# Kernel optimization log

Hardware: AMD Instinct MI355X
Metric: run time of the kernel (lower is better)

The kernel has to match this reference:

```python
import jax, jax.numpy as jnp
import numpy as np

B, T, C, H = 2, 2048, 1024, 16
HS = C // H  # 64
EPS = 1e-5


def layer_norm(x, w, b):
    mu = jnp.mean(x, axis=-1, keepdims=True)
    var = jnp.var(x, axis=-1, keepdims=True)
    return (x - mu) * jax.lax.rsqrt(var + EPS) * w + b


def setup_inputs() -> dict:
    key = jax.random.key(0)
    ks = jax.random.split(key, 16)
    s_c = 1.0 / np.sqrt(C)
    s_f = 1.0 / np.sqrt(4 * C)
    u = lambda k, shape, s: jax.random.uniform(k, shape, jnp.float32, -s, s)
    return {
        "x": jax.random.normal(ks[0], (B, T, C), jnp.float32),
        # per-head Q/K/V Linears stacked over heads: [H, C, HS], bias [H, HS]
        "Wq": u(ks[1], (H, C, HS), s_c), "bq": u(ks[2], (H, HS), s_c),
        "Wk": u(ks[3], (H, C, HS), s_c), "bk": u(ks[4], (H, HS), s_c),
        "Wv": u(ks[5], (H, C, HS), s_c), "bv": u(ks[6], (H, HS), s_c),
        "Wp": u(ks[7], (C, C), s_c), "bp": u(ks[8], (C,), s_c),
        "W1": u(ks[9], (C, 4 * C), s_c), "b1": u(ks[10], (4 * C,), s_c),
        "W2": u(ks[11], (4 * C, C), s_f), "b2": u(ks[12], (C,), s_f),
        "ln1_w": jnp.ones((C,), jnp.float32), "ln1_b": jnp.zeros((C,), jnp.float32),
        "ln2_w": jnp.ones((C,), jnp.float32), "ln2_b": jnp.zeros((C,), jnp.float32),
    }


def reference(x, Wq, bq, Wk, bk, Wv, bv, Wp, bp, W1, b1, W2, b2,
              ln1_w, ln1_b, ln2_w, ln2_b):
    # --- pre-norm self-attention ---
    xn = layer_norm(x, ln1_w, ln1_b)
    q = jnp.einsum('btc,hcd->bhtd', xn, Wq) + bq[None, :, None, :]
    k = jnp.einsum('btc,hcd->bhtd', xn, Wk) + bk[None, :, None, :]
    v = jnp.einsum('btc,hcd->bhtd', xn, Wv) + bv[None, :, None, :]
    # NOTE: original scales by C**-0.5 (full embedding dim), not head_size**-0.5
    att = jnp.einsum('bhtd,bhsd->bhts', q, k) * (C ** -0.5)
    att = jax.nn.softmax(att, axis=-1)
    o = jnp.einsum('bhts,bhsd->bhtd', att, v)  # [B,H,T,HS]
    o = jnp.transpose(o, (0, 2, 1, 3)).reshape(B, T, C)  # concat heads
    sa = o @ Wp + bp
    out = x + sa
    # --- pre-norm FFN (exact erf GELU, matching nn.GELU default) ---
    on = layer_norm(out, ln2_w, ln2_b)
    h = jax.nn.gelu(on @ W1 + b1, approximate=False)
    return out + (h @ W2 + b2)
```

## Files before the change

kernel.cpp:

```cpp
#include <hip/hip_runtime.h>
#include <math.h>

#define BB 2
#define TT 2048
#define CC 1024
#define HH 16
#define HS 64
#define MT 4096
#define FF 4096

typedef unsigned short u16;
typedef __bf16 bfrag __attribute__((ext_vector_type(8)));
typedef float f4 __attribute__((ext_vector_type(4)));

#define AS1(p) ((const __attribute__((address_space(1))) void*)(p))
#define AS3(p) ((__attribute__((address_space(3))) void*)(p))

__device__ __forceinline__ u16 f2bf(float f) {
  union { float f; unsigned u; } a; a.f = f;
  return (u16)((a.u + 0x7fffu + ((a.u >> 16) & 1u)) >> 16);
}

__device__ __forceinline__ int swz128(int byteoff) {
  return byteoff ^ (((byteoff >> 7) & 7) << 4);
}

__device__ __forceinline__ int swzAB(int byteoff) {
  return byteoff ^ (((byteoff >> 7) & 3) << 4);
}

__global__ void tr_f32_bf16(const float* __restrict__ src, u16* __restrict__ dst,
                            int R, int Cc, long long sb, long long db, int dld) {
  __shared__ float t[32][33];
  const int bz = blockIdx.z;
  const int r0 = blockIdx.y * 32, c0 = blockIdx.x * 32;
  const int tx = threadIdx.x, ty = threadIdx.y;
  const float* s = src + bz * sb;
  u16* d = dst + bz * db;
#pragma unroll
  for (int i = 0; i < 4; i++)
    t[ty + i * 8][tx] = s[(size_t)(r0 + ty + i * 8) * Cc + c0 + tx];
  __syncthreads();
#pragma unroll
  for (int i = 0; i < 4; i++)
    d[(size_t)(c0 + ty + i * 8) * dld + r0 + tx] = f2bf(t[tx][ty + i * 8]);
}

__global__ void tr_bf16(const u16* __restrict__ src, u16* __restrict__ dst,
                        int R, int Cc, long long sb, long long db, int dld) {
  __shared__ u16 t[32][33];
  const int bz = blockIdx.z;
  const int r0 = blockIdx.y * 32, c0 = blockIdx.x * 32;
  const int tx = threadIdx.x, ty = threadIdx.y;
  const u16* s = src + bz * sb;
  u16* d = dst + bz * db;
#pragma unroll
  for (int i = 0; i < 4; i++)
    t[ty + i * 8][tx] = s[(size_t)(r0 + ty + i * 8) * Cc + c0 + tx];
  __syncthreads();
#pragma unroll
  for (int i = 0; i < 4; i++)
    d[(size_t)(c0 + ty + i * 8) * dld + r0 + tx] = t[tx][ty + i * 8];
}

__global__ __launch_bounds__(256) void ln_kernel(
    const float* __restrict__ x, const float* __restrict__ w,
    const float* __restrict__ b, u16* __restrict__ y) {
  const int row = blockIdx.x, tid = threadIdx.x;
  const float4 v = reinterpret_cast<const float4*>(x + (size_t)row * CC)[tid];
  float s = v.x + v.y + v.z + v.w;
  float s2 = v.x * v.x + v.y * v.y + v.z * v.z + v.w * v.w;
#pragma unroll
  for (int off = 32; off >= 1; off >>= 1) {
    s += __shfl_xor(s, off);
    s2 += __shfl_xor(s2, off);
  }
  __shared__ float ps[4], ps2[4];
  const int wave = tid >> 6, lane = tid & 63;
  if (lane == 0) { ps[wave] = s; ps2[wave] = s2; }
  __syncthreads();
  s = ps[0] + ps[1] + ps[2] + ps[3];
  s2 = ps2[0] + ps2[1] + ps2[2] + ps2[3];
  const float mu = s * (1.f / CC);
  const float rstd = rsqrtf(s2 * (1.f / CC) - mu * mu + 1e-5f);
  const float4 wv = reinterpret_cast<const float4*>(w)[tid];
  const float4 bv = reinterpret_cast<const float4*>(b)[tid];
  ushort4 o;
  o.x = f2bf((v.x - mu) * rstd * wv.x + bv.x);
  o.y = f2bf((v.y - mu) * rstd * wv.y + bv.y);
  o.z = f2bf((v.z - mu) * rstd * wv.z + bv.z);
  o.w = f2bf((v.w - mu) * rstd * wv.w + bv.w);
  reinterpret_cast<ushort4*>(y + (size_t)row * CC)[tid] = o;
}

template<int NJ>
__device__ __forceinline__ void gemm_core(
    const u16* __restrict__ A, const u16* __restrict__ Bt, int K,
    f4 (&acc)[4][NJ]) {
  constexpr int BN = NJ * 32;
  __shared__ u16 As[3][128 * 32];
  __shared__ u16 Bs[3][BN * 32];
  const int tid = threadIdx.x;
  const int wave = tid >> 6, lane = tid & 63;
  const int wm = wave >> 1, wn = wave & 1;
  const int lg = lane >> 4, ll = lane & 15;

  const int trow = tid >> 2;
  const int tch  = (tid & 3) ^ ((trow >> 1) & 3);
  const u16* ga = A + (size_t)(blockIdx.y * 128 + trow) * K + tch * 8;
  const u16* gb = Bt + (size_t)(blockIdx.x * BN + trow) * K + tch * 8;
  const size_t g64 = (size_t)64 * K;
  const int nt = K >> 5;

  auto GSTAGE = [&](int bi, int kt) {
    u16* la = &As[bi][tid * 8];
    u16* lb = &Bs[bi][tid * 8];
    const u16* gA = ga + kt * 32;
    const u16* gB = gb + kt * 32;
    __builtin_amdgcn_global_load_lds(AS1(gA), AS3(la), 16, 0, 0);
    __builtin_amdgcn_global_load_lds(AS1(gA + g64), AS3(la + 2048), 16, 0, 0);
    __builtin_amdgcn_global_load_lds(AS1(gB), AS3(lb), 16, 0, 0);
    if constexpr (NJ == 4)
      __builtin_amdgcn_global_load_lds(AS1(gB + g64), AS3(lb + 2048), 16, 0, 0);
  };

  GSTAGE(0, 0);
  GSTAGE(1, 1);
  GSTAGE(2, 2);
  int bi = 0;
  for (int t = 0; t < nt; t++) {
    const int ahead = nt - 1 - t;
    if constexpr (NJ == 4) {
      if (ahead >= 2)      asm volatile("s_waitcnt vmcnt(8)" ::: "memory");
      else if (ahead == 1) asm volatile("s_waitcnt vmcnt(4)" ::: "memory");
      else                 asm volatile("s_waitcnt vmcnt(0)" ::: "memory");
    } else {
      if (ahead >= 2)      asm volatile("s_waitcnt vmcnt(6)" ::: "memory");
      else if (ahead == 1) asm volatile("s_waitcnt vmcnt(3)" ::: "memory");
      else                 asm volatile("s_waitcnt vmcnt(0)" ::: "memory");
    }
    __builtin_amdgcn_s_barrier();
    __builtin_amdgcn_sched_barrier(0);

    const char* as_ = (const char*)As[bi];
    const char* bs_ = (const char*)Bs[bi];
    bfrag af[4], bf[NJ];
#pragma unroll
    for (int i = 0; i < 4; i++)
      af[i] = *(const bfrag*)(as_ + swzAB((wm * 64 + i * 16 + ll) * 64 + lg * 16));
#pragma unroll
    for (int j = 0; j < NJ; j++)
      bf[j] = *(const bfrag*)(bs_ + swzAB((wn * (BN / 2) + j * 16 + ll) * 64 + lg * 16));

    __builtin_amdgcn_s_setprio(1);
#pragma unroll
    for (int i = 0; i < 4; i++)
#pragma unroll
      for (int j = 0; j < NJ; j++)
        acc[i][j] = __builtin_amdgcn_mfma_f32_16x16x32_bf16(af[i], bf[j], acc[i][j], 0, 0, 0);
    __builtin_amdgcn_s_setprio(0);

    __builtin_amdgcn_sched_barrier(0);
    __builtin_amdgcn_s_barrier();
    if (t + 3 < nt) GSTAGE(bi, t + 3);
    bi = (bi == 2) ? 0 : bi + 1;
  }
}

#define EPI_COORDS                                              \
  const int tid = threadIdx.x;                                  \
  const int wave = tid >> 6, lane = tid & 63;                   \
  const int wm = wave >> 1, wn = wave & 1;                      \
  const int lg = lane >> 4, ll = lane & 15;

__global__ __launch_bounds__(256, 2) void gemm_qkv(
    const u16* __restrict__ A, const u16* __restrict__ Bt,
    const float* __restrict__ bq, const float* __restrict__ bk,
    const float* __restrict__ bv,
    u16* __restrict__ q, u16* __restrict__ k, u16* __restrict__ v) {
  f4 acc[4][4] = {};
  gemm_core<4>(A, Bt, CC, acc);
  EPI_COORDS
#pragma unroll
  for (int j = 0; j < 4; j++) {
    const int n = blockIdx.x * 128 + wn * 64 + j * 16 + ll;
    const int sec = n >> 10, nn = n & 1023, h = nn >> 6, d = nn & 63;
    const float bias = (sec == 0 ? bq : (sec == 1 ? bk : bv))[nn];
    const float scale = (sec == 0) ? 0.03125f : 1.0f;
    u16* dst = sec == 0 ? q : (sec == 1 ? k : v);
#pragma unroll
    for (int i = 0; i < 4; i++)
#pragma unroll
      for (int r = 0; r < 4; r++) {
        const int m = blockIdx.y * 128 + wm * 64 + i * 16 + lg * 4 + r;
        const int b = m >> 11, t = m & 2047;
        dst[(((size_t)b * HH + h) * TT + t) * HS + d] = f2bf((acc[i][j][r] + bias) * scale);
      }
  }
}

__global__ __launch_bounds__(256, 2) void gemm_proj(
    const u16* __restrict__ A, const u16* __restrict__ Bt,
    const float* __restrict__ bp, const float* __restrict__ x,
    float* __restrict__ outw) {
  f4 acc[4][2] = {};
  gemm_core<2>(A, Bt, CC, acc);
  EPI_COORDS
#pragma unroll
  for (int i = 0; i < 4; i++)
#pragma unroll
    for (int j = 0; j < 2; j++) {
      const int n = blockIdx.x * 64 + wn * 32 + j * 16 + ll;
      const float bias = bp[n];
#pragma unroll
      for (int r = 0; r < 4; r++) {
        const int m = blockIdx.y * 128 + wm * 64 + i * 16 + lg * 4 + r;
        const size_t idx = (size_t)m * CC + n;
        outw[idx] = acc[i][j][r] + bias + x[idx];
      }
    }
}

__global__ __launch_bounds__(256, 2) void gemm_ffn1(
    const u16* __restrict__ A, const u16* __restrict__ Bt,
    const float* __restrict__ b1, u16* __restrict__ hb) {
  f4 acc[4][4] = {};
  gemm_core<4>(A, Bt, CC, acc);
  EPI_COORDS
#pragma unroll
  for (int i = 0; i < 4; i++)
#pragma unroll
    for (int j = 0; j < 4; j++) {
      const int n = blockIdx.x * 128 + wn * 64 + j * 16 + ll;
      const float bias = b1[n];
#pragma unroll
      for (int r = 0; r < 4; r++) {
        const int m = blockIdx.y * 128 + wm * 64 + i * 16 + lg * 4 + r;
        const float t = acc[i][j][r] + bias;
        const float g = 0.5f * t * (1.0f + erff(t * 0.70710678118654752f));
        hb[(size_t)m * FF + n] = f2bf(g);
      }
    }
}

__global__ __launch_bounds__(256, 2) void gemm_ffn2(
    const u16* __restrict__ A, const u16* __restrict__ Bt,
    const float* __restrict__ b2, const float* __restrict__ outw,
    float* __restrict__ dout) {
  f4 acc[4][2] = {};
  gemm_core<2>(A, Bt, FF, acc);
  EPI_COORDS
#pragma unroll
  for (int i = 0; i < 4; i++)
#pragma unroll
    for (int j = 0; j < 2; j++) {
      const int n = blockIdx.x * 64 + wn * 32 + j * 16 + ll;
      const float bias = b2[n];
#pragma unroll
      for (int r = 0; r < 4; r++) {
        const int m = blockIdx.y * 128 + wm * 64 + i * 16 + lg * 4 + r;
        const size_t idx = (size_t)m * CC + n;
        dout[idx] = acc[i][j][r] + bias + outw[idx];
      }
    }
}

__global__ __launch_bounds__(256, 2) void attn_kernel(
    const u16* __restrict__ Q, const u16* __restrict__ Kb,
    const u16* __restrict__ Vt, u16* __restrict__ Ao) {
  __shared__ __align__(1024) u16 Ks[2][64 * 64];
  __shared__ __align__(1024) u16 Vs[2][64 * 64];
  __shared__ __align__(1024) u16 Ps[4][32 * 64];
  const int bh = blockIdx.y, qt = blockIdx.x;
  const int tid = threadIdx.x, wave = tid >> 6, lane = tid & 63;
  const int lg = lane >> 4, ll = lane & 15;

  bfrag qf[2][2];
  const u16* Qb = Q + ((size_t)bh * TT + qt * 128 + wave * 32) * HS;
#pragma unroll
  for (int qb = 0; qb < 2; qb++)
#pragma unroll
    for (int dc = 0; dc < 2; dc++)
      qf[qb][dc] = *(const bfrag*)&Qb[(qb * 16 + ll) * HS + dc * 32 + lg * 8];

  f4 o[2][4] = {};
  float mrun[2] = {-INFINITY, -INFINITY}, lrun[2] = {0.f, 0.f};

  const int trow = tid >> 3;
  const int tch  = (tid & 7) ^ (trow & 7);
  const u16* gk = Kb + ((size_t)bh * TT + trow) * HS + tch * 8;
  const u16* gv = Vt + ((size_t)bh * HS + trow) * TT + tch * 8;

  char* const pw = (char*)Ps[wave];

#define STAGE(bufi, stt)                                                          \
  do {                                                                            \
    u16* lk = &Ks[bufi][tid * 8];                                                 \
    u16* lv = &Vs[bufi][tid * 8];                                                 \
    __builtin_amdgcn_global_load_lds(AS1(gk + (size_t)(stt) * HS), AS3(lk), 16, 0, 0); \
    __builtin_amdgcn_global_load_lds(AS1(gk + (size_t)(stt) * HS + 32 * HS), AS3(lk + 2048), 16, 0, 0); \
    __builtin_amdgcn_global_load_lds(AS1(gv + (stt)), AS3(lv), 16, 0, 0);         \
    __builtin_amdgcn_global_load_lds(AS1(gv + (stt) + (size_t)32 * TT), AS3(lv + 2048), 16, 0, 0); \
  } while (0)

  STAGE(0, 0);
  int cur = 0;

  for (int st = 0; st < TT; st += 64) {
    if (st + 64 < TT) {
      STAGE(cur ^ 1, st + 64);
      asm volatile("s_waitcnt vmcnt(4)" ::: "memory");
    } else {
      asm volatile("s_waitcnt vmcnt(0)" ::: "memory");
    }
    __builtin_amdgcn_s_barrier();
    __builtin_amdgcn_sched_barrier(0);

    const char* kbuf = (const char*)Ks[cur];
    const char* vbuf = (const char*)Vs[cur];

    f4 p[2][4];
#pragma unroll
    for (int kb = 0; kb < 4; kb++) {
      const int row = kb * 16 + ll;
      const bfrag k0 = *(const bfrag*)(kbuf + swz128(row * 128 + lg * 16));
      const bfrag k1 = *(const bfrag*)(kbuf + swz128(row * 128 + 64 + lg * 16));
#pragma unroll
      for (int qb = 0; qb < 2; qb++) {
        f4 z = {0.f, 0.f, 0.f, 0.f};
        z = __builtin_amdgcn_mfma_f32_16x16x32_bf16(k0, qf[qb][0], z, 0, 0, 0);
        p[qb][kb] = __builtin_amdgcn_mfma_f32_16x16x32_bf16(k1, qf[qb][1], z, 0, 0, 0);
      }
    }

#pragma unroll
    for (int qb = 0; qb < 2; qb++) {
      float pm = p[qb][0][0];
#pragma unroll
      for (int kb = 0; kb < 4; kb++)
#pragma unroll
        for (int r = 0; r < 4; r++)
          if (kb | r) pm = fmaxf(pm, p[qb][kb][r]);
      pm = fmaxf(pm, __shfl_xor(pm, 16));
      pm = fmaxf(pm, __shfl_xor(pm, 32));
      const float mn = fmaxf(mrun[qb], pm);
      const float al = __expf(mrun[qb] - mn);
      mrun[qb] = mn;
      float rs = 0.f;
#pragma unroll
      for (int kb = 0; kb < 4; kb++)
#pragma unroll
        for (int r = 0; r < 4; r++) {
          const float e = __expf(p[qb][kb][r] - mn);
          p[qb][kb][r] = e;
          rs += e;
        }
      rs += __shfl_xor(rs, 16);
      rs += __shfl_xor(rs, 32);
      lrun[qb] = lrun[qb] * al + rs;
#pragma unroll
      for (int fo = 0; fo < 4; fo++) o[qb][fo] *= al;
#pragma unroll
      for (int kb = 0; kb < 4; kb++) {
        union { uint2 v; __bf16 h[4]; } w;
        w.h[0] = (__bf16)p[qb][kb][0];
        w.h[1] = (__bf16)p[qb][kb][1];
        w.h[2] = (__bf16)p[qb][kb][2];
        w.h[3] = (__bf16)p[qb][kb][3];
        *(uint2*)(pw + swz128((qb * 16 + ll) * 128 + kb * 32 + lg * 8)) = w.v;
      }
    }

#pragma unroll
    for (int ks = 0; ks < 2; ks++) {
      const bfrag pb0 = *(const bfrag*)(pw + swz128(ll * 128 + ks * 64 + lg * 16));
      const bfrag pb1 = *(const bfrag*)(pw + swz128((16 + ll) * 128 + ks * 64 + lg * 16));
#pragma unroll
      for (int fo = 0; fo < 4; fo++) {
        const bfrag vf = *(const bfrag*)(vbuf + swz128((fo * 16 + ll) * 128 + ks * 64 + lg * 16));
        o[0][fo] = __builtin_amdgcn_mfma_f32_16x16x32_bf16(vf, pb0, o[0][fo], 0, 0, 0);
        o[1][fo] = __builtin_amdgcn_mfma_f32_16x16x32_bf16(vf, pb1, o[1][fo], 0, 0, 0);
      }
    }

    __builtin_amdgcn_sched_barrier(0);
    __builtin_amdgcn_s_barrier();
    cur ^= 1;
  }
#undef STAGE

  const int b = bh >> 4, h = bh & 15;
#pragma unroll
  for (int qb = 0; qb < 2; qb++) {
    const float inv = 1.0f / lrun[qb];
    const int t = qt * 128 + wave * 32 + qb * 16 + ll;
#pragma unroll
    for (int fo = 0; fo < 4; fo++) {
      union { uint2 v; __bf16 h[4]; } w;
      w.h[0] = (__bf16)(o[qb][fo][0] * inv);
      w.h[1] = (__bf16)(o[qb][fo][1] * inv);
      w.h[2] = (__bf16)(o[qb][fo][2] * inv);
      w.h[3] = (__bf16)(o[qb][fo][3] * inv);
      *(uint2*)&Ao[((size_t)b * TT + t) * CC + h * HS + fo * 16 + lg * 4] = w.v;
    }
  }
}

extern "C" void kernel_launch(void* const* d_in, const int* in_sizes, int n_in,
                              void* d_out, int out_size, void* d_ws, size_t ws_size,
                              hipStream_t stream) {
  const float* x    = (const float*)d_in[0];
  const float* Wq   = (const float*)d_in[1];
  const float* bq   = (const float*)d_in[2];
  const float* Wk   = (const float*)d_in[3];
  const float* bk   = (const float*)d_in[4];
  const float* Wv   = (const float*)d_in[5];
  const float* bv   = (const float*)d_in[6];
  const float* Wp   = (const float*)d_in[7];
  const float* bp   = (const float*)d_in[8];
  const float* W1   = (const float*)d_in[9];
  const float* b1   = (const float*)d_in[10];
  const float* W2   = (const float*)d_in[11];
  const float* b2   = (const float*)d_in[12];
  const float* ln1w = (const float*)d_in[13];
  const float* ln1b = (const float*)d_in[14];
  const float* ln2w = (const float*)d_in[15];
  const float* ln2b = (const float*)d_in[16];
  float* dout = (float*)d_out;

  char* ws = (char*)d_ws;
  u16* wqkv = (u16*)(ws + 0);
  u16* wpt  = (u16*)(ws + 6291456);
  u16* w1t  = (u16*)(ws + 8388608);
  u16* w2t  = (u16*)(ws + 16777216);
  u16* xn   = (u16*)(ws + 25165824);
  u16* qb   = (u16*)(ws + 33554432);
  u16* kb   = (u16*)(ws + 41943040);
  u16* vb   = (u16*)(ws + 50331648);
  u16* vt   = (u16*)(ws + 58720256);
  u16* ao   = (u16*)(ws + 67108864);
  u16* hb   = qb;

  dim3 blk256(256);
  dim3 blkT(32, 8);

  tr_f32_bf16<<<dim3(2, 32, 16), blkT, 0, stream>>>(Wq, wqkv,               1024,   64, 65536LL, 65536LL, 1024);
  tr_f32_bf16<<<dim3(2, 32, 16), blkT, 0, stream>>>(Wk, wqkv + 1024 * 1024, 1024,   64, 65536LL, 65536LL, 1024);
  tr_f32_bf16<<<dim3(2, 32, 16), blkT, 0, stream>>>(Wv, wqkv + 2048 * 1024, 1024,   64, 65536LL, 65536LL, 1024);
  tr_f32_bf16<<<dim3(32, 32, 1),  blkT, 0, stream>>>(Wp, wpt, 1024, 1024, 0LL, 0LL, 1024);
  tr_f32_bf16<<<dim3(128, 32, 1), blkT, 0, stream>>>(W1, w1t, 1024, 4096, 0LL, 0LL, 1024);
  tr_f32_bf16<<<dim3(32, 128, 1), blkT, 0, stream>>>(W2, w2t, 4096, 1024, 0LL, 0LL, 4096);

  ln_kernel<<<dim3(MT), blk256, 0, stream>>>(x, ln1w, ln1b, xn);

  gemm_qkv<<<dim3(24, 32), blk256, 0, stream>>>(xn, wqkv, bq, bk, bv, qb, kb, vb);

  tr_bf16<<<dim3(2, 64, 32), blkT, 0, stream>>>(vb, vt, 2048, 64, 131072LL, 131072LL, 2048);

  attn_kernel<<<dim3(16, 32), blk256, 0, stream>>>(qb, kb, vt, ao);

  gemm_proj<<<dim3(16, 32), blk256, 0, stream>>>(ao, wpt, bp, x, dout);

  ln_kernel<<<dim3(MT), blk256, 0, stream>>>(dout, ln2w, ln2b, xn);

  gemm_ffn1<<<dim3(32, 32), blk256, 0, stream>>>(xn, w1t, b1, hb);
  gemm_ffn2<<<dim3(16, 32), blk256, 0, stream>>>(hb, w2t, b2, dout, dout);
}
```

Before: 292.0 us.

## Split-K FFN2, LDS-staged epilogues, XCD block swizzle, and exp2-based softmax

Replaces the FFN2 GEMM with a two-way split-K kernel using 128x128 tiles that writes bf16 partials, plus a separate reduce kernel that adds bias and residual. The QKV and FFN1 epilogues now stage results through shared memory so global stores are 16-byte coalesced rows. A block-index remap spreads neighbouring tiles across XCDs, and launch bounds are raised to allow three blocks per CU. Attention folds log2(e) into the Q scale so softmax can use exp2f. The bf16 partial sums and the extra reduce pass add rounding error and memory traffic in exchange for more parallelism.

```diff
diff --git a/kernel.cpp b/kernel.cpp
--- a/kernel.cpp
+++ b/kernel.cpp
@@ -20,14 +20,23 @@
   union { float f; unsigned u; } a; a.f = f;
   return (u16)((a.u + 0x7fffu + ((a.u >> 16) & 1u)) >> 16);
 }
+__device__ __forceinline__ float bf2f(u16 u) {
+  union { unsigned u; float f; } a; a.u = ((unsigned)u) << 16; return a.f;
+}
 
 __device__ __forceinline__ int swz128(int byteoff) {
   return byteoff ^ (((byteoff >> 7) & 7) << 4);
 }
-
 __device__ __forceinline__ int swzAB(int byteoff) {
   return byteoff ^ (((byteoff >> 7) & 3) << 4);
 }
+
+#define XCD_SWZ_2D(BX, BY)                                                     \
+  int _fl = (int)blockIdx.y * gridDim.x + blockIdx.x;                          \
+  const int _nw = gridDim.x * gridDim.y;                                       \
+  _fl = (_fl & 7) * (_nw >> 3) + (_fl >> 3);                                   \
+  const int BX = _fl % gridDim.x;                                              \
+  const int BY = _fl / gridDim.x;
 
 __global__ void tr_f32_bf16(const float* __restrict__ src, u16* __restrict__ dst,
                             int R, int Cc, long long sb, long long db, int dld) {
@@ -95,11 +104,12 @@
 
 template<int NJ>
 __device__ __forceinline__ void gemm_core(
-    const u16* __restrict__ A, const u16* __restrict__ Bt, int K,
-    f4 (&acc)[4][NJ]) {
+    u16* smem, const u16* __restrict__ A, const u16* __restrict__ Bt,
+    int K, int lda, int ldb, int bmi, int bni, f4 (&acc)[4][NJ]) {
   constexpr int BN = NJ * 32;
-  __shared__ u16 As[3][128 * 32];
-  __shared__ u16 Bs[3][BN * 32];
+  constexpr int BBUF = BN * 32;
+  u16* As = smem;
+  u16* Bs = smem + 3 * 4096;
   const int tid = threadIdx.x;
   const int wave = tid >> 6, lane = tid & 63;
   const int wm = wave >> 1, wn = wave & 1;
@@ -107,21 +117,22 @@
 
   const int trow = tid >> 2;
   const int tch  = (tid & 3) ^ ((trow >> 1) & 3);
-  const u16* ga = A + (size_t)(blockIdx.y * 128 + trow) * K + tch * 8;
-  const u16* gb = Bt + (size_t)(blockIdx.x * BN + trow) * K + tch * 8;
-  const size_t g64 = (size_t)64 * K;
+  const u16* ga = A + (size_t)(bmi * 128 + trow) * lda + tch * 8;
+  const u16* gb = Bt + (size_t)(bni * BN + trow) * ldb + tch * 8;
+  const size_t g64a = (size_t)64 * lda;
+  const size_t g64b = (size_t)64 * ldb;
   const int nt = K >> 5;
 
   auto GSTAGE = [&](int bi, int kt) {
-    u16* la = &As[bi][tid * 8];
-    u16* lb = &Bs[bi][tid * 8];
+    u16* la = &As[bi * 4096 + tid * 8];
+    u16* lb = &Bs[bi * BBUF + tid * 8];
     const u16* gA = ga + kt * 32;
     const u16* gB = gb + kt * 32;
     __builtin_amdgcn_global_load_lds(AS1(gA), AS3(la), 16, 0, 0);
-    __builtin_amdgcn_global_load_lds(AS1(gA + g64), AS3(la + 2048), 16, 0, 0);
+    __builtin_amdgcn_global_load_lds(AS1(gA + g64a), AS3(la + 2048), 16, 0, 0);
     __builtin_amdgcn_global_load_lds(AS1(gB), AS3(lb), 16, 0, 0);
     if constexpr (NJ == 4)
-      __builtin_amdgcn_global_load_lds(AS1(gB + g64), AS3(lb + 2048), 16, 0, 0);
+      __builtin_amdgcn_global_load_lds(AS1(gB + g64b), AS3(lb + 2048), 16, 0, 0);
   };
 
   GSTAGE(0, 0);
@@ -142,8 +153,8 @@
     __builtin_amdgcn_s_barrier();
     __builtin_amdgcn_sched_barrier(0);
 
-    const char* as_ = (const char*)As[bi];
-    const char* bs_ = (const char*)Bs[bi];
+    const char* as_ = (const char*)(As + bi * 4096);
+    const char* bs_ = (const char*)(Bs + bi * BBUF);
     bfrag af[4], bf[NJ];
 #pragma unroll
     for (int i = 0; i < 4; i++)
@@ -173,94 +184,155 @@
   const int wm = wave >> 1, wn = wave & 1;                      \
   const int lg = lane >> 4, ll = lane & 15;
 
-__global__ __launch_bounds__(256, 2) void gemm_qkv(
+__global__ __launch_bounds__(256, 3) void gemm_qkv(
     const u16* __restrict__ A, const u16* __restrict__ Bt,
     const float* __restrict__ bq, const float* __restrict__ bk,
     const float* __restrict__ bv,
     u16* __restrict__ q, u16* __restrict__ k, u16* __restrict__ v) {
+  __shared__ u16 smem[24576];
+  XCD_SWZ_2D(bx, by)
   f4 acc[4][4] = {};
-  gemm_core<4>(A, Bt, CC, acc);
+  gemm_core<4>(smem, A, Bt, CC, CC, CC, by, bx, acc);
   EPI_COORDS
+  __syncthreads();
 #pragma unroll
   for (int j = 0; j < 4; j++) {
-    const int n = blockIdx.x * 128 + wn * 64 + j * 16 + ll;
+    const int n = bx * 128 + wn * 64 + j * 16 + ll;
+    const int sec = n >> 10, nn = n & 1023;
+    const float bias = (sec == 0 ? bq : (sec == 1 ? bk : bv))[nn];
+    const float scale = (sec == 0) ? 0.045084220027780106f : 1.0f;
+#pragma unroll
+    for (int i = 0; i < 4; i++)
+#pragma unroll
+      for (int r = 0; r < 4; r++)
+        smem[(wm * 64 + i * 16 + lg * 4 + r) * 136 + wn * 64 + j * 16 + ll] =
+            f2bf((acc[i][j][r] + bias) * scale);
+  }
+  __syncthreads();
+  const int rr = tid >> 4, cb = (tid & 15) * 8;
+#pragma unroll
+  for (int R = 0; R < 8; R++) {
+    const int row = R * 16 + rr;
+    const int m = by * 128 + row, b = m >> 11, t = m & 2047;
+    const int n = bx * 128 + cb;
     const int sec = n >> 10, nn = n & 1023, h = nn >> 6, d = nn & 63;
-    const float bias = (sec == 0 ? bq : (sec == 1 ? bk : bv))[nn];
-    const float scale = (sec == 0) ? 0.03125f : 1.0f;
     u16* dst = sec == 0 ? q : (sec == 1 ? k : v);
+    *(uint4*)&dst[(((size_t)b * HH + h) * TT + t) * HS + d] =
+        *(const uint4*)&smem[row * 136 + cb];
+  }
+}
+
+__global__ __launch_bounds__(256, 3) void gemm_ffn1(
+    const u16* __restrict__ A, const u16* __restrict__ Bt,
+    const float* __restrict__ b1, u16* __restrict__ hb) {
+  __shared__ u16 smem[24576];
+  XCD_SWZ_2D(bx, by)
+  f4 acc[4][4] = {};
+  gemm_core<4>(smem, A, Bt, CC, CC, CC, by, bx, acc);
+  EPI_COORDS
+  __syncthreads();
+#pragma unroll
+  for (int j = 0; j < 4; j++) {
+    const int n = bx * 128 + wn * 64 + j * 16 + ll;
+    const float bias = b1[n];
 #pragma unroll
     for (int i = 0; i < 4; i++)
 #pragma unroll
       for (int r = 0; r < 4; r++) {
-        const int m = blockIdx.y * 128 + wm * 64 + i * 16 + lg * 4 + r;
-        const int b = m >> 11, t = m & 2047;
-        dst[(((size_t)b * HH + h) * TT + t) * HS + d] = f2bf((acc[i][j][r] + bias) * scale);
+        const float t = acc[i][j][r] + bias;
+        const float g = 0.5f * t * (1.0f + erff(t * 0.70710678118654752f));
+        smem[(wm * 64 + i * 16 + lg * 4 + r) * 136 + wn * 64 + j * 16 + ll] = f2bf(g);
       }
   }
-}
-
-__global__ __launch_bounds__(256, 2) void gemm_proj(
+  __syncthreads();
+  const int rr = tid >> 4, cb = (tid & 15) * 8;
+#pragma unroll
+  for (int R = 0; R < 8; R++) {
+    const int row = R * 16 + rr;
+    *(uint4*)&hb[(size_t)(by * 128 + row) * FF + bx * 128 + cb] =
+        *(const uint4*)&smem[row * 136 + cb];
+  }
+}
+
+__global__ __launch_bounds__(256, 3) void gemm_ffn2sk(
+    const u16* __restrict__ A, const u16* __restrict__ Bt,
+    u16* __restrict__ p0, u16* __restrict__ p1) {
+  __shared__ u16 smem[24576];
+  int _fl = ((int)blockIdx.z * gridDim.y + blockIdx.y) * gridDim.x + blockIdx.x;
+  const int _nw = gridDim.x * gridDim.y * gridDim.z;
+  _fl = (_fl & 7) * (_nw >> 3) + (_fl >> 3);
+  const int bx = _fl % gridDim.x;
+  const int by = (_fl / gridDim.x) % gridDim.y;
+  const int bz = _fl / (gridDim.x * gridDim.y);
+
+  f4 acc[4][4] = {};
+  gemm_core<4>(smem, A + bz * 2048, Bt + bz * 2048, 2048, FF, FF, by, bx, acc);
+  EPI_COORDS
+  __syncthreads();
+#pragma unroll
+  for (int j = 0; j < 4; j++)
+#pragma unroll
+    for (int i = 0; i < 4; i++)
+#pragma unroll
+      for (int r = 0; r < 4; r++)
+        smem[(wm * 64 + i * 16 + lg * 4 + r) * 136 + wn * 64 + j * 16 + ll] =
+            f2bf(acc[i][j][r]);
+  __syncthreads();
+  u16* pp = bz ? p1 : p0;
+  const int rr = tid >> 4, cb = (tid & 15) * 8;
+#pragma unroll
+  for (int R = 0; R < 8; R++) {
+    const int row = R * 16 + rr;
+    *(uint4*)&pp[(size_t)(by * 128 + row) * CC + bx * 128 + cb] =
+        *(const uint4*)&smem[row * 136 + cb];
+  }
+}
+
+__global__ __launch_bounds__(256) void ffn2_reduce(
+    const u16* __restrict__ p0, const u16* __restrict__ p1,
+    const float* __restrict__ b2, float* __restrict__ dout) {
+  const int gid = blockIdx.x * 256 + threadIdx.x;
+  const int n0 = (gid * 8) & (CC - 1);
+  const uint4 a = ((const uint4*)p0)[gid];
+  const uint4 c = ((const uint4*)p1)[gid];
+  const u16* au = (const u16*)&a;
+  const u16* cu = (const u16*)&c;
+  float4 d0 = ((const float4*)dout)[gid * 2];
+  float4 d1 = ((const float4*)dout)[gid * 2 + 1];
+  const float4 w0 = *(const float4*)&b2[n0];
+  const float4 w1 = *(const float4*)&b2[n0 + 4];
+  d0.x += w0.x + bf2f(au[0]) + bf2f(cu[0]);
+  d0.y += w0.y + bf2f(au[1]) + bf2f(cu[1]);
+  d0.z += w0.z + bf2f(au[2]) + bf2f(cu[2]);
+  d0.w += w0.w + bf2f(au[3]) + bf2f(cu[3]);
+  d1.x += w1.x + bf2f(au[4]) + bf2f(cu[4]);
+  d1.y += w1.y + bf2f(au[5]) + bf2f(cu[5]);
+  d1.z += w1.z + bf2f(au[6]) + bf2f(cu[6]);
+  d1.w += w1.w + bf2f(au[7]) + bf2f(cu[7]);
+  ((float4*)dout)[gid * 2] = d0;
+  ((float4*)dout)[gid * 2 + 1] = d1;
+}
+
+__global__ __launch_bounds__(256, 3) void gemm_proj(
     const u16* __restrict__ A, const u16* __restrict__ Bt,
     const float* __restrict__ bp, const float* __restrict__ x,
     float* __restrict__ outw) {
+  __shared__ u16 smem[18432];
+  XCD_SWZ_2D(bx, by)
   f4 acc[4][2] = {};
-  gemm_core<2>(A, Bt, CC, acc);
+  gemm_core<2>(smem, A, Bt, CC, CC, CC, by, bx, acc);
   EPI_COORDS
 #pragma unroll
   for (int i = 0; i < 4; i++)
 #pragma unroll
     for (int j = 0; j < 2; j++) {
-      const int n = blockIdx.x * 64 + wn * 32 + j * 16 + ll;
+      const int n = bx * 64 + wn * 32 + j * 16 + ll;
       const float bias = bp[n];
 #pragma unroll
       for (int r = 0; r < 4; r++) {
-        const int m = blockIdx.y * 128 + wm * 64 + i * 16 + lg * 4 + r;
+        const int m = by * 128 + wm * 64 + i * 16 + lg * 4 + r;
         const size_t idx = (size_t)m * CC + n;
         outw[idx] = acc[i][j][r] + bias + x[idx];
-      }
-    }
-}
-
-__global__ __launch_bounds__(256, 2) void gemm_ffn1(
-    const u16* __restrict__ A, const u16* __restrict__ Bt,
-    const float* __restrict__ b1, u16* __restrict__ hb) {
-  f4 acc[4][4] = {};
-  gemm_core<4>(A, Bt, CC, acc);
-  EPI_COORDS
-#pragma unroll
-  for (int i = 0; i < 4; i++)
-#pragma unroll
-    for (int j = 0; j < 4; j++) {
-      const int n = blockIdx.x * 128 + wn * 64 + j * 16 + ll;
-      const float bias = b1[n];
-#pragma unroll
-      for (int r = 0; r < 4; r++) {
-        const int m = blockIdx.y * 128 + wm * 64 + i * 16 + lg * 4 + r;
-        const float t = acc[i][j][r] + bias;
-        const float g = 0.5f * t * (1.0f + erff(t * 0.70710678118654752f));
-        hb[(size_t)m * FF + n] = f2bf(g);
-      }
-    }
-}
-
-__global__ __launch_bounds__(256, 2) void gemm_ffn2(
-    const u16* __restrict__ A, const u16* __restrict__ Bt,
-    const float* __restrict__ b2, const float* __restrict__ outw,
-    float* __restrict__ dout) {
-  f4 acc[4][2] = {};
-  gemm_core<2>(A, Bt, FF, acc);
-  EPI_COORDS
-#pragma unroll
-  for (int i = 0; i < 4; i++)
-#pragma unroll
-    for (int j = 0; j < 2; j++) {
-      const int n = blockIdx.x * 64 + wn * 32 + j * 16 + ll;
-      const float bias = b2[n];
-#pragma unroll
-      for (int r = 0; r < 4; r++) {
-        const int m = blockIdx.y * 128 + wm * 64 + i * 16 + lg * 4 + r;
-        const size_t idx = (size_t)m * CC + n;
-        dout[idx] = acc[i][j][r] + bias + outw[idx];
       }
     }
 }
@@ -344,14 +416,14 @@
       pm = fmaxf(pm, __shfl_xor(pm, 16));
       pm = fmaxf(pm, __shfl_xor(pm, 32));
       const float mn = fmaxf(mrun[qb], pm);
-      const float al = __expf(mrun[qb] - mn);
+      const float al = exp2f(mrun[qb] - mn);
       mrun[qb] = mn;
       float rs = 0.f;
 #pragma unroll
       for (int kb = 0; kb < 4; kb++)
 #pragma unroll
         for (int r = 0; r < 4; r++) {
-          const float e = __expf(p[qb][kb][r] - mn);
+          const float e = exp2f(p[qb][kb][r] - mn);
           p[qb][kb][r] = e;
           rs += e;
         }
@@ -440,6 +512,8 @@
   u16* vt   = (u16*)(ws + 58720256);
   u16* ao   = (u16*)(ws + 67108864);
   u16* hb   = qb;
+  u16* pk0  = (u16*)(ws + 0);
+  u16* pk1  = (u16*)(ws + 8388608);
 
   dim3 blk256(256);
   dim3 blkT(32, 8);
@@ -464,5 +538,6 @@
   ln_kernel<<<dim3(MT), blk256, 0, stream>>>(dout, ln2w, ln2b, xn);
 
   gemm_ffn1<<<dim3(32, 32), blk256, 0, stream>>>(xn, w1t, b1, hb);
-  gemm_ffn2<<<dim3(16, 32), blk256, 0, stream>>>(hb, w2t, b2, dout, dout);
-}
+  gemm_ffn2sk<<<dim3(8, 32, 2), blk256, 0, stream>>>(hb, w2t, pk0, pk1);
+  ffn2_reduce<<<dim3(MT * CC / 8 / 256), blk256, 0, stream>>>(pk0, pk1, b2, dout);
+}
```

New measurement: 279.6 us. -4.3%, faster.
